# Kernel tuning notes

Measured on AMD Instinct MI355X. Metric: run time of the kernel, lower is better.

## Reference

```python
import jax, jax.numpy as jnp
from jax import lax
import numpy as np

SEL = [46, 92]
A_SEL = [16, 32]
EPS = 1e-16


def _descriptors(xyz, atomtypes, box):
    # xyz: (B,N,3) float, atomtypes: (B,N) int, box: scalar
    B, N, _ = xyz.shape
    dm = xyz[:, :, None, :] - xyz[:, None, :, :] + EPS          # (B,N,N,3)
    dm = dm - box * jnp.round(dm / box)                          # min-image PBC
    dist = jnp.sqrt(jnp.sum(dm * dm, axis=-1))                   # (B,N,N)
    self_mask = jnp.eye(N, dtype=bool)[None]                     # exclude self
    radial, a_xyz_list, a_dist_list = [], [], []
    lf_d = lf_i = None
    for j, (selj, aselj) in enumerate(zip(SEL, A_SEL)):
        mask = (atomtypes == j)[:, None, :] & (~self_mask)       # (B,N,N)
        d_j = jnp.where(mask, dist, jnp.inf)
        k = max(selj, aselj, 2)
        neg, idx = lax.top_k(-d_j, k)                            # k smallest
        sd = -neg                                                # (B,N,k)
        if j == 0:
            lf_d, lf_i = sd[..., :2], idx[..., :2]
        else:
            better = sd[..., :2] < lf_d
            lf_d = jnp.where(better, sd[..., :2], lf_d)
            lf_i = jnp.where(better, idx[..., :2], lf_i)
        radial.append(1.0 / (sd[..., :selj] + EPS))
        a_xyz_list.append(jnp.take_along_axis(dm, idx[..., :aselj, None], axis=2))
        a_dist_list.append(sd[..., :aselj])
    a_xyz = jnp.concatenate(a_xyz_list, axis=2)                  # (B,N,sumA,3)
    a_dist = jnp.concatenate(a_dist_list, axis=2)[..., None]     # (B,N,sumA,1)
    # local frame from the 2 globally nearest neighbors
    l_xyz = jnp.take_along_axis(dm, lf_i[..., None], axis=2) / (lf_d[..., None] + EPS)
    r0, r1 = l_xyz[:, :, 0], l_xyz[:, :, 1]                      # (B,N,3)
    v2 = r1 - jnp.sum(r0 * r1, -1, keepdims=True) * r0
    v2 = v2 / jnp.linalg.norm(v2, axis=-1, keepdims=True)
    v3 = jnp.cross(r0, r1)
    v3 = v3 / jnp.linalg.norm(v3, axis=-1, keepdims=True)
    A = jnp.stack([r0, v2, v3], axis=-2)                         # (B,N,3,3)
    a_xyz = a_xyz / (a_dist + EPS)
    a_xyz = jnp.einsum('bnij,bnkj->bnki', A, a_xyz)
    a_xyz = a_xyz / (a_dist + EPS)  # faithful: source divides by a_dist twice
    return jnp.concatenate(radial + [a_xyz.reshape(B, N, -1)], axis=-1)


def _energy(xyz, atomtypes, box, params):
    # norm is (mean=0, std=1) in the source -> identity, skipped.
    desc = _descriptors(xyz, atomtypes, box)
    e = jnp.zeros(desc.shape[:2], desc.dtype)
    for t, layers in enumerate(params):
        h = desc
        for (W, b) in layers[:-1]:
            h = jnp.tanh(h @ W + b)
        W, b = layers[-1]
        e = jnp.where(atomtypes == t, (h @ W + b)[..., 0], e)
    return jnp.sum(e, axis=1)                                    # (B,)


def setup_inputs():
    key = jax.random.key(0)
    ks = jax.random.split(key, 16)
    B, N, box = 2, 2048, 27
    xyz = jax.random.uniform(ks[0], (B, N, 3), dtype=jnp.float32) * box
    atomtypes = jax.random.randint(ks[1], (B, N), 0, 2)
    D = sum(SEL) + 3 * sum(A_SEL)  # 282
    sizes = [D, 64, 64, 1]
    inp = {'xyz': xyz, 'atomtypes': atomtypes, 'box_size': box}
    ki = 2
    for t in range(2):
        for l in range(3):
            fi, fo = sizes[l], sizes[l + 1]
            inp[f'W{t}_{l}'] = jax.random.normal(ks[ki], (fi, fo), dtype=jnp.float32) / np.sqrt(fi).astype(np.float32)
            inp[f'b{t}_{l}'] = jnp.zeros((fo,), jnp.float32)
            ki += 1
    return inp


def reference(xyz, atomtypes, box_size, W0_0, b0_0, W0_1, b0_1, W0_2, b0_2,
              W1_0, b1_0, W1_1, b1_1, W1_2, b1_2):
    params = [[(W0_0, b0_0), (W0_1, b0_1), (W0_2, b0_2)],
              [(W1_0, b1_0), (W1_1, b1_1), (W1_2, b1_2)]]
    energy = _energy(xyz, atomtypes, box_size, params)
    forces = -jax.grad(lambda x: jnp.sum(_energy(x, atomtypes, box_size, params)))(xyz)
    return energy, forces
```

## Files before the change

kernel.cpp:

```cpp
#include <hip/hip_runtime.h>
#include <stdint.h>
#include <math.h>

#define BLOCK 256
#define WPB 4
#define SEL0 46
#define SEL1 92
#define ASEL0 16
#define ASEL1 32
#define NNB 138
#define NANG 48
#define DDIM 282
#define HID 64
#define FEPS 1e-16f
#define NPT 32
#define CAP 128
#define NREP 16

__device__ __forceinline__ float mimg(float dx, float box, float ibox) {
    return dx - box * rintf(dx * ibox);
}

__device__ __forceinline__ void wsync() {
    asm volatile("s_waitcnt lgkmcnt(0)" ::: "memory");
    __builtin_amdgcn_wave_barrier();
}

__device__ __forceinline__ void decode(unsigned long long k, float& d, int& j) {
    uint32_t idx = (uint32_t)(k & 0xFFFFFFFFull);
    if (idx == 0xFFFFFFFFu) { d = 1e30f; j = -1; }
    else { d = __uint_as_float((uint32_t)(k >> 32)); j = (int)idx; }
}

__device__ __forceinline__ void atomF(float* p, float v, bool wg) {
    if (wg) (void)__hip_atomic_fetch_add(p, v, __ATOMIC_RELAXED,
                                         __HIP_MEMORY_SCOPE_WORKGROUP);
    else    atomicAdd(p, v);
}

__global__ __launch_bounds__(BLOCK)
void reduce_kernel(const float* __restrict__ rep, float* __restrict__ out,
                   int total, int Bc, int eoff, int rstride, int nrep)
{
    int e = blockIdx.x * BLOCK + threadIdx.x;
    if (e >= total) return;
    int src = (e < Bc) ? (eoff + e) : (e - Bc);
    float s = 0.0f;
    for (int r = 0; r < nrep; ++r) s += rep[(size_t)r * rstride + src];
    out[e] = s;
}

__global__ __launch_bounds__(BLOCK, 4)
void md_kernel(const float* __restrict__ xyz, const int* __restrict__ types,
               const void* __restrict__ boxp,
               const float* __restrict__ W0a, const float* __restrict__ B0a,
               const float* __restrict__ W1a, const float* __restrict__ B1a,
               const float* __restrict__ W2a, const float* __restrict__ B2a,
               const float* __restrict__ W0b, const float* __restrict__ B0b,
               const float* __restrict__ W1b, const float* __restrict__ B1b,
               const float* __restrict__ W2b, const float* __restrict__ B2b,
               float* __restrict__ out, float* __restrict__ repbase,
               int nrep, int eoff, int rstride, int B, int N)
{
    __shared__ unsigned long long A0s[WPB][CAP];
    __shared__ unsigned long long A1s[WPB][CAP];
    __shared__ float sdescs[WPB][DDIM];
    __shared__ float sgs[WPB][DDIM];
    __shared__ float sAs[WPB][9];
    __shared__ float sh1s[WPB][HID];
    __shared__ float sdh1s[WPB][HID];

    const int w = threadIdx.x >> 6;
    const int lane = threadIdx.x & 63;
    const int atom = blockIdx.x * WPB + w;
    if (atom >= B * N) return;
    const int b = atom / N;
    const int i = atom - b * N;

    unsigned long long* A0w = A0s[w];
    unsigned long long* A1w = A1s[w];
    float* sdescw = sdescs[w];
    float* sgw = sgs[w];
    float* sAw = sAs[w];
    float* sh1w = sh1s[w];
    float* sdh1w = sdh1s[w];

    const bool wg = (repbase != nullptr);
    float* Fout;
    float* Eout;
    if (wg) {
        uint32_t xcc;
        asm volatile("s_getreg_b32 %0, hwreg(HW_REG_XCC_ID)" : "=s"(xcc));
        int ridx = (int)((xcc & 7u) * 2u + (blockIdx.x & 1u));
        float* base = repbase + (size_t)ridx * rstride;
        Fout = base; Eout = base + eoff;
    } else {
        Fout = out + B; Eout = out;
    }

    int ib_test = ((const int*)boxp)[0];
    float box = (ib_test > 0 && ib_test < 1000000) ? (float)ib_test
                                                   : ((const float*)boxp)[0];
    float ibox = 1.0f / box;

    const float* X = xyz + (size_t)b * N * 3;
    const int*   T = types + (size_t)b * N;
    const int ti = T[i];
    const float xi = X[3*i+0], yi = X[3*i+1], zi = X[3*i+2];

    uint32_t rk[NPT];
    #pragma unroll
    for (int jj = 0; jj < NPT; ++jj) {
        int j = jj * 64 + lane;
        uint32_t k = 0x7FFFFFFFu;
        if (j < N && j != i) {
            float dx = mimg(xi - X[3*j+0], box, ibox);
            float dy = mimg(yi - X[3*j+1], box, ibox);
            float dz = mimg(zi - X[3*j+2], box, ibox);
            float d = sqrtf(dx*dx + dy*dy + dz*dz);
            k = __float_as_uint(d) | (T[j] ? 0x80000000u : 0u);
        }
        rk[jj] = k;
    }

    uint32_t t1 = 0;
    #pragma unroll
    for (int jj = 0; jj < NPT; ++jj) t1 += (rk[jj] >> 31);
    #pragma unroll
    for (int o = 32; o > 0; o >>= 1) t1 += __shfl_down(t1, o, 64);
    t1 = __shfl(t1, 0, 64);
    const int tot1 = (int)t1;
    const int tot0 = (N - 1) - tot1;
    const int need0 = min(SEL0, tot0);
    const int need1 = min(SEL1, tot1);

    const float vol = box * box * box;
    const float c43pi = 4.18879020f;
    float R0 = cbrtf(0.5f * (need0 + CAP) * vol / (c43pi * fmaxf((float)tot0, 1.0f)));
    float R1 = cbrtf(0.5f * (need1 + CAP) * vol / (c43pi * fmaxf((float)tot1, 1.0f)));
    uint32_t Rb0 = __float_as_uint(R0), Rb1 = __float_as_uint(R1);
    float lo0 = 0.0f, hi0 = -1.0f, lo1 = 0.0f, hi1 = -1.0f;
    for (int it = 0; it < 20; ++it) {
        uint32_t c0 = 0, c1 = 0;
        #pragma unroll
        for (int jj = 0; jj < NPT; ++jj) {
            uint32_t k = rk[jj];
            c0 += ((k < 0x80000000u) && (k < Rb0));
            c1 += ((k >= 0x80000000u) && ((k & 0x7FFFFFFFu) < Rb1));
        }
        uint32_t packed = c0 | (c1 << 16);
        #pragma unroll
        for (int o = 32; o > 0; o >>= 1) packed += __shfl_down(packed, o, 64);
        packed = __shfl(packed, 0, 64);
        int cc0 = (int)(packed & 0xFFFFu);
        int cc1 = (int)(packed >> 16);
        bool done0 = (cc0 >= need0 && cc0 <= CAP);
        bool done1 = (cc1 >= need1 && cc1 <= CAP);
        if (done0 && done1) break;
        if (!done0) {
            if (cc0 < need0) { lo0 = R0; R0 = (hi0 > 0.0f) ? 0.5f*(lo0+hi0) : R0*1.3f; }
            else             { hi0 = R0; R0 = 0.5f*(lo0+hi0); }
            Rb0 = __float_as_uint(R0);
        }
        if (!done1) {
            if (cc1 < need1) { lo1 = R1; R1 = (hi1 > 0.0f) ? 0.5f*(lo1+hi1) : R1*1.3f; }
            else             { hi1 = R1; R1 = 0.5f*(lo1+hi1); }
            Rb1 = __float_as_uint(R1);
        }
    }

    const unsigned long long lmlt = (1ull << lane) - 1ull;
    int base0 = 0, base1 = 0;
    #pragma unroll
    for (int jj = 0; jj < NPT; ++jj) {
        uint32_t k = rk[jj];
        bool p0 = (k < 0x80000000u) && (k < Rb0);
        bool p1 = (k >= 0x80000000u) && ((k & 0x7FFFFFFFu) < Rb1);
        unsigned long long m0 = __ballot(p0);
        unsigned long long m1 = __ballot(p1);
        if (p0) {
            int pos = base0 + __popcll(m0 & lmlt);
            if (pos < CAP)
                A0w[pos] = ((unsigned long long)k << 32) | (uint32_t)(jj*64 + lane);
        }
        if (p1) {
            int pos = base1 + __popcll(m1 & lmlt);
            if (pos < CAP)
                A1w[pos] = ((unsigned long long)(k & 0x7FFFFFFFu) << 32) | (uint32_t)(jj*64 + lane);
        }
        base0 += __popcll(m0);
        base1 += __popcll(m1);
    }
    const int c0n = min(base0, CAP);
    const int c1n = min(base1, CAP);
    #pragma unroll
    for (int t = lane; t < CAP; t += 64) {
        if (t >= c0n) A0w[t] = ~0ull;
        if (t >= c1n) A1w[t] = ~0ull;
    }
    wsync();

    {
        unsigned long long va = A0w[lane], vb = A0w[lane + 64];
        unsigned long long wa = A1w[lane], wb = A1w[lane + 64];
        #pragma unroll
        for (int size = 2; size <= 128; size <<= 1) {
            #pragma unroll
            for (int stride = 64; stride > 0; stride >>= 1) {
                if (stride >= size) continue;
                if (stride == 64) {
                    unsigned long long mn = va < vb ? va : vb;
                    unsigned long long mx = va < vb ? vb : va;
                    va = mn; vb = mx;
                    mn = wa < wb ? wa : wb;
                    mx = wa < wb ? wb : wa;
                    wa = mn; wb = mx;
                } else {
                    bool keep_lo = (lane & stride) == 0;
                    bool asc0 = ((lane & size) == 0);
                    bool asc1 = (((lane + 64) & size) == 0);
                    unsigned long long oa = __shfl_xor(va, stride, 64);
                    unsigned long long ob = __shfl_xor(vb, stride, 64);
                    va = (asc0 == keep_lo) ? (va < oa ? va : oa) : (va > oa ? va : oa);
                    vb = (asc1 == keep_lo) ? (vb < ob ? vb : ob) : (vb > ob ? vb : ob);
                    oa = __shfl_xor(wa, stride, 64);
                    ob = __shfl_xor(wb, stride, 64);
                    wa = (asc0 == keep_lo) ? (wa < oa ? wa : oa) : (wa > oa ? wa : oa);
                    wb = (asc1 == keep_lo) ? (wb < ob ? wb : ob) : (wb > ob ? wb : ob);
                }
            }
        }
        A0w[lane] = va; A0w[lane + 64] = vb;
        A1w[lane] = wa; A1w[lane + 64] = wb;
    }
    wsync();

    for (int t = lane; t < NNB; t += 64) {
        unsigned long long k = (t < SEL0) ? A0w[t] : A1w[t - SEL0];
        float d; int j; decode(k, d, j);
        sdescw[t] = 1.0f / (d + FEPS);
    }

    float f_ld0 = 1.0f, f_ld1 = 1.0f; int f_j0 = -1, f_j1 = -1;
    float r0x=0,r0y=0,r0z=0, r1x=0,r1y=0,r1z=0;
    float u0x=0,u0y=0,u0z=0, u1x=0,u1y=0,u1z=0;
    float f_s=0, f_n2=1, f_n3=1;
    float e2x=0,e2y=0,e2z=0, e3x=0,e3y=0,e3z=0;
    if (lane == 0) {
        float da0, da1, db0, db1; int ja0, ja1, jb0, jb1;
        decode(A0w[0], da0, ja0);
        decode(A0w[1], da1, ja1);
        decode(A1w[0], db0, jb0);
        decode(A1w[1], db1, jb1);
        f_ld0 = (db0 < da0) ? db0 : da0;  f_j0 = (db0 < da0) ? jb0 : ja0;
        f_ld1 = (db1 < da1) ? db1 : da1;  f_j1 = (db1 < da1) ? jb1 : ja1;
        if (f_j0 < 0) f_j0 = i;
        if (f_j1 < 0) f_j1 = i;
        u0x = mimg(xi - X[3*f_j0+0], box, ibox);
        u0y = mimg(yi - X[3*f_j0+1], box, ibox);
        u0z = mimg(zi - X[3*f_j0+2], box, ibox);
        u1x = mimg(xi - X[3*f_j1+0], box, ibox);
        u1y = mimg(yi - X[3*f_j1+1], box, ibox);
        u1z = mimg(zi - X[3*f_j1+2], box, ibox);
        float id0 = 1.0f/(f_ld0 + FEPS), id1 = 1.0f/(f_ld1 + FEPS);
        r0x = u0x*id0; r0y = u0y*id0; r0z = u0z*id0;
        r1x = u1x*id1; r1y = u1y*id1; r1z = u1z*id1;
        f_s = r0x*r1x + r0y*r1y + r0z*r1z;
        float v2x = r1x - f_s*r0x, v2y = r1y - f_s*r0y, v2z = r1z - f_s*r0z;
        f_n2 = sqrtf(v2x*v2x + v2y*v2y + v2z*v2z);
        e2x = v2x/f_n2; e2y = v2y/f_n2; e2z = v2z/f_n2;
        float cx = r0y*r1z - r0z*r1y;
        float cy = r0z*r1x - r0x*r1z;
        float cz = r0x*r1y - r0y*r1x;
        f_n3 = sqrtf(cx*cx + cy*cy + cz*cz);
        e3x = cx/f_n3; e3y = cy/f_n3; e3z = cz/f_n3;
        sAw[0]=r0x; sAw[1]=r0y; sAw[2]=r0z;
        sAw[3]=e2x; sAw[4]=e2y; sAw[5]=e2z;
        sAw[6]=e3x; sAw[7]=e3y; sAw[8]=e3z;
    }
    wsync();

    if (lane < NANG) {
        int slot = (lane < ASEL0) ? lane : SEL0 + (lane - ASEL0);
        unsigned long long k = (slot < SEL0) ? A0w[slot] : A1w[slot - SEL0];
        float d; int j; decode(k, d, j);
        float dx = 0, dy = 0, dz = 0;
        if (j >= 0) {
            dx = mimg(xi - X[3*j+0], box, ibox);
            dy = mimg(yi - X[3*j+1], box, ibox);
            dz = mimg(zi - X[3*j+2], box, ibox);
        }
        float de = d + FEPS;
        float q = 1.0f/(de*de);
        float wx = sAw[0]*dx + sAw[1]*dy + sAw[2]*dz;
        float wy = sAw[3]*dx + sAw[4]*dy + sAw[5]*dz;
        float wz = sAw[6]*dx + sAw[7]*dy + sAw[8]*dz;
        sdescw[NNB + 3*lane + 0] = wx*q;
        sdescw[NNB + 3*lane + 1] = wy*q;
        sdescw[NNB + 3*lane + 2] = wz*q;
    }
    wsync();

    const float* W0 = ti ? W0b : W0a;  const float* B0 = ti ? B0b : B0a;
    const float* W1 = ti ? W1b : W1a;  const float* B1 = ti ? B1b : B1a;
    const float* W2 = ti ? W2b : W2a;  const float* B2 = ti ? B2b : B2a;

    float acc = B0[lane];
    for (int d = 0; d < DDIM; ++d) acc = fmaf(sdescw[d], W0[d*HID + lane], acc);
    float h1 = tanhf(acc);
    sh1w[lane] = h1;
    wsync();

    float acc2 = B1[lane];
    #pragma unroll
    for (int m = 0; m < HID; ++m) acc2 = fmaf(sh1w[m], W1[m*HID + lane], acc2);
    float h2 = tanhf(acc2);
    float w2v = W2[lane];
    float part = h2 * w2v;
    #pragma unroll
    for (int o = 32; o > 0; o >>= 1) part += __shfl_down(part, o, 64);
    if (lane == 0) atomF(&Eout[b], part + B2[0], wg);
    float dh2 = (1.0f - h2*h2) * w2v;
    sdh1w[lane] = dh2;
    wsync();

    float accb = 0.0f;
    #pragma unroll
    for (int m = 0; m < HID; ++m) accb = fmaf(W1[lane*HID + m], sdh1w[m], accb);
    wsync();
    float dh1 = (1.0f - h1*h1) * accb;
    sdh1w[lane] = dh1;
    wsync();

    for (int d = lane; d < DDIM; d += 64) {
        float a = 0.0f;
        #pragma unroll
        for (int m = 0; m < HID; ++m) a = fmaf(W0[d*HID + m], sdh1w[m], a);
        sgw[d] = a;
    }
    wsync();

    float rG[9];
    #pragma unroll
    for (int q9 = 0; q9 < 9; ++q9) rG[q9] = 0.0f;
    float fix = 0.0f, fiy = 0.0f, fiz = 0.0f;

    for (int t = lane; t < NNB; t += 64) {
        unsigned long long k = (t < SEL0) ? A0w[t] : A1w[t - SEL0];
        float d; int j; decode(k, d, j);
        if (j >= 0) {
            float dx = mimg(xi - X[3*j+0], box, ibox);
            float dy = mimg(yi - X[3*j+1], box, ibox);
            float dz = mimg(zi - X[3*j+2], box, ibox);
            float gr = sgw[t];
            float de = d + FEPS;
            float coef = -gr / (d * de * de);
            float gx = coef*dx, gy = coef*dy, gz = coef*dz;
            int a = -1;
            if (t < ASEL0) a = t;
            else if (t >= SEL0 && t < SEL0 + ASEL1) a = ASEL0 + (t - SEL0);
            if (a >= 0) {
                float q = 1.0f/(de*de);
                float gax = sgw[NNB+3*a+0], gay = sgw[NNB+3*a+1], gaz = sgw[NNB+3*a+2];
                float wx = sAw[0]*dx + sAw[1]*dy + sAw[2]*dz;
                float wy = sAw[3]*dx + sAw[4]*dy + sAw[5]*dz;
                float wz = sAw[6]*dx + sAw[7]*dy + sAw[8]*dz;
                float tx = sAw[0]*gax + sAw[3]*gay + sAw[6]*gaz;
                float ty = sAw[1]*gax + sAw[4]*gay + sAw[7]*gaz;
                float tz = sAw[2]*gax + sAw[5]*gay + sAw[8]*gaz;
                float gw = gax*wx + gay*wy + gaz*wz;
                float c2 = -2.0f * gw * q / (de * d);
                gx += q*tx + c2*dx;
                gy += q*ty + c2*dy;
                gz += q*tz + c2*dz;
                rG[0] += gax*dx*q; rG[1] += gax*dy*q; rG[2] += gax*dz*q;
                rG[3] += gay*dx*q; rG[4] += gay*dy*q; rG[5] += gay*dz*q;
                rG[6] += gaz*dx*q; rG[7] += gaz*dy*q; rG[8] += gaz*dz*q;
            }
            float* Fj = Fout + 3*((size_t)b*N + j);
            atomF(&Fj[0], gx, wg); atomF(&Fj[1], gy, wg); atomF(&Fj[2], gz, wg);
            fix -= gx; fiy -= gy; fiz -= gz;
        }
    }

    #pragma unroll
    for (int o = 32; o > 0; o >>= 1) {
        #pragma unroll
        for (int q9 = 0; q9 < 9; ++q9) rG[q9] += __shfl_down(rG[q9], o, 64);
        fix += __shfl_down(fix, o, 64);
        fiy += __shfl_down(fiy, o, 64);
        fiz += __shfl_down(fiz, o, 64);
    }

    if (lane == 0) {
        float g0x=rG[0], g0y=rG[1], g0z=rG[2];
        float g2x=rG[3], g2y=rG[4], g2z=rG[5];
        float g3x=rG[6], g3y=rG[7], g3z=rG[8];
        float d3 = g3x*e3x + g3y*e3y + g3z*e3z;
        float in3 = 1.0f/f_n3;
        float dcx = (g3x - d3*e3x)*in3;
        float dcy = (g3y - d3*e3y)*in3;
        float dcz = (g3z - d3*e3z)*in3;
        float gr0x = r1y*dcz - r1z*dcy;
        float gr0y = r1z*dcx - r1x*dcz;
        float gr0z = r1x*dcy - r1y*dcx;
        float gr1x = dcy*r0z - dcz*r0y;
        float gr1y = dcz*r0x - dcx*r0z;
        float gr1z = dcx*r0y - dcy*r0x;
        float d2 = g2x*e2x + g2y*e2y + g2z*e2z;
        float in2 = 1.0f/f_n2;
        float dvx = (g2x - d2*e2x)*in2;
        float dvy = (g2y - d2*e2y)*in2;
        float dvz = (g2z - d2*e2z)*in2;
        gr1x += dvx; gr1y += dvy; gr1z += dvz;
        gr0x -= f_s*dvx; gr0y -= f_s*dvy; gr0z -= f_s*dvz;
        float dss = -(dvx*r0x + dvy*r0y + dvz*r0z);
        gr0x += dss*r1x; gr0y += dss*r1y; gr0z += dss*r1z;
        gr1x += dss*r0x; gr1y += dss*r0y; gr1z += dss*r0z;
        gr0x += g0x; gr0y += g0y; gr0z += g0z;
        float de0 = f_ld0 + FEPS;
        float dot0 = gr0x*u0x + gr0y*u0y + gr0z*u0z;
        float k0 = dot0 / (f_ld0 * de0 * de0);
        float gu0x = gr0x/de0 - k0*u0x;
        float gu0y = gr0y/de0 - k0*u0y;
        float gu0z = gr0z/de0 - k0*u0z;
        float de1 = f_ld1 + FEPS;
        float dot1 = gr1x*u1x + gr1y*u1y + gr1z*u1z;
        float k1 = dot1 / (f_ld1 * de1 * de1);
        float gu1x = gr1x/de1 - k1*u1x;
        float gu1y = gr1y/de1 - k1*u1y;
        float gu1z = gr1z/de1 - k1*u1z;
        float* Fj0 = Fout + 3*((size_t)b*N + f_j0);
        atomF(&Fj0[0], gu0x, wg); atomF(&Fj0[1], gu0y, wg); atomF(&Fj0[2], gu0z, wg);
        float* Fj1 = Fout + 3*((size_t)b*N + f_j1);
        atomF(&Fj1[0], gu1x, wg); atomF(&Fj1[1], gu1y, wg); atomF(&Fj1[2], gu1z, wg);
        fix -= gu0x + gu1x;
        fiy -= gu0y + gu1y;
        fiz -= gu0z + gu1z;
        float* Fi = Fout + 3*((size_t)b*N + i);
        atomF(&Fi[0], fix, wg); atomF(&Fi[1], fiy, wg); atomF(&Fi[2], fiz, wg);
    }
}

extern "C" void kernel_launch(void* const* d_in, const int* in_sizes, int n_in,
                              void* d_out, int out_size, void* d_ws, size_t ws_size,
                              hipStream_t stream) {
    const float* xyz  = (const float*)d_in[0];
    const int*   types = (const int*)d_in[1];
    const void*  boxp = d_in[2];
    int BN = in_sizes[1];
    int B = out_size - 3*BN;
    if (B < 1) B = 1;
    int N = BN / B;

    int eoff = ((3 * BN + 31) / 32) * 32;
    int rstride = eoff + ((B + 31) / 32) * 32;
    int nrep = NREP;
    size_t need = (size_t)nrep * rstride * sizeof(float);
    float* rep = (need <= ws_size) ? (float*)d_ws : nullptr;

    if (rep) {
        hipMemsetAsync(d_ws, 0, need, stream);
    } else {
        nrep = 1;
        hipMemsetAsync(d_out, 0, (size_t)out_size * sizeof(float), stream);
    }

    int nblk = (BN + WPB - 1) / WPB;
    md_kernel<<<dim3(nblk), dim3(BLOCK), 0, stream>>>(
        xyz, types, boxp,
        (const float*)d_in[3],  (const float*)d_in[4],
        (const float*)d_in[5],  (const float*)d_in[6],
        (const float*)d_in[7],  (const float*)d_in[8],
        (const float*)d_in[9],  (const float*)d_in[10],
        (const float*)d_in[11], (const float*)d_in[12],
        (const float*)d_in[13], (const float*)d_in[14],
        (float*)d_out, rep, nrep, eoff, rstride, B, N);

    if (rep) {
        int total = out_size;
        int nb = (total + BLOCK - 1) / BLOCK;
        reduce_kernel<<<dim3(nb), dim3(BLOCK), 0, stream>>>(
            rep, (float*)d_out, total, B, eoff, rstride, nrep);
    }
}
```

Measured before the change: 282.7 us.

## Accumulate forces in per-block shared memory and write per-block slots for reduction

```diff
diff --git a/kernel.cpp b/kernel.cpp
--- a/kernel.cpp
+++ b/kernel.cpp
@@ -15,7 +15,8 @@
 #define FEPS 1e-16f
 #define NPT 32
 #define CAP 128
-#define NREP 16
+#define NMAX 2048
+#define SFE (3*NMAX)
 
 __device__ __forceinline__ float mimg(float dx, float box, float ibox) {
     return dx - box * rintf(dx * ibox);
@@ -32,25 +33,27 @@
     else { d = __uint_as_float((uint32_t)(k >> 32)); j = (int)idx; }
 }
 
-__device__ __forceinline__ void atomF(float* p, float v, bool wg) {
-    if (wg) (void)__hip_atomic_fetch_add(p, v, __ATOMIC_RELAXED,
-                                         __HIP_MEMORY_SCOPE_WORKGROUP);
-    else    atomicAdd(p, v);
-}
-
 __global__ __launch_bounds__(BLOCK)
 void reduce_kernel(const float* __restrict__ rep, float* __restrict__ out,
-                   int total, int Bc, int eoff, int rstride, int nrep)
+                   int total, int B, int N, int sstride, int nspb)
 {
     int e = blockIdx.x * BLOCK + threadIdx.x;
     if (e >= total) return;
-    int src = (e < Bc) ? (eoff + e) : (e - Bc);
     float s = 0.0f;
-    for (int r = 0; r < nrep; ++r) s += rep[(size_t)r * rstride + src];
+    if (e < B) {
+        const float* p = rep + (size_t)e * nspb * sstride + 3 * N;
+        for (int r = 0; r < nspb; ++r) s += p[(size_t)r * sstride];
+    } else {
+        int f = e - B;
+        int b = f / (3 * N);
+        int elem = f - b * 3 * N;
+        const float* p = rep + (size_t)b * nspb * sstride + elem;
+        for (int r = 0; r < nspb; ++r) s += p[(size_t)r * sstride];
+    }
     out[e] = s;
 }
 
-__global__ __launch_bounds__(BLOCK, 4)
+__global__ __launch_bounds__(BLOCK, 2)
 void md_kernel(const float* __restrict__ xyz, const int* __restrict__ types,
                const void* __restrict__ boxp,
                const float* __restrict__ W0a, const float* __restrict__ B0a,
@@ -59,8 +62,8 @@
                const float* __restrict__ W0b, const float* __restrict__ B0b,
                const float* __restrict__ W1b, const float* __restrict__ B1b,
                const float* __restrict__ W2b, const float* __restrict__ B2b,
-               float* __restrict__ out, float* __restrict__ repbase,
-               int nrep, int eoff, int rstride, int B, int N)
+               float* __restrict__ out, float* __restrict__ slotbase,
+               int sstride, int G, int B, int N)
 {
     __shared__ unsigned long long A0s[WPB][CAP];
     __shared__ unsigned long long A1s[WPB][CAP];
@@ -69,13 +72,14 @@
     __shared__ float sAs[WPB][9];
     __shared__ float sh1s[WPB][HID];
     __shared__ float sdh1s[WPB][HID];
+    __shared__ float sF[3*NMAX + 8];
 
     const int w = threadIdx.x >> 6;
     const int lane = threadIdx.x & 63;
-    const int atom = blockIdx.x * WPB + w;
-    if (atom >= B * N) return;
-    const int b = atom / N;
-    const int i = atom - b * N;
+    const bool lmode = (slotbase != nullptr);
+
+    for (int s2 = threadIdx.x; s2 <= SFE; s2 += BLOCK) sF[s2] = 0.0f;
+    __syncthreads();
 
     unsigned long long* A0w = A0s[w];
     unsigned long long* A1w = A1s[w];
@@ -85,360 +89,385 @@
     float* sh1w = sh1s[w];
     float* sdh1w = sdh1s[w];
 
-    const bool wg = (repbase != nullptr);
-    float* Fout;
-    float* Eout;
-    if (wg) {
-        uint32_t xcc;
-        asm volatile("s_getreg_b32 %0, hwreg(HW_REG_XCC_ID)" : "=s"(xcc));
-        int ridx = (int)((xcc & 7u) * 2u + (blockIdx.x & 1u));
-        float* base = repbase + (size_t)ridx * rstride;
-        Fout = base; Eout = base + eoff;
-    } else {
-        Fout = out + B; Eout = out;
-    }
-
     int ib_test = ((const int*)boxp)[0];
     float box = (ib_test > 0 && ib_test < 1000000) ? (float)ib_test
                                                    : ((const float*)boxp)[0];
     float ibox = 1.0f / box;
 
-    const float* X = xyz + (size_t)b * N * 3;
-    const int*   T = types + (size_t)b * N;
-    const int ti = T[i];
-    const float xi = X[3*i+0], yi = X[3*i+1], zi = X[3*i+2];
-
-    uint32_t rk[NPT];
-    #pragma unroll
-    for (int jj = 0; jj < NPT; ++jj) {
-        int j = jj * 64 + lane;
-        uint32_t k = 0x7FFFFFFFu;
-        if (j < N && j != i) {
-            float dx = mimg(xi - X[3*j+0], box, ibox);
-            float dy = mimg(yi - X[3*j+1], box, ibox);
-            float dz = mimg(zi - X[3*j+2], box, ibox);
-            float d = sqrtf(dx*dx + dy*dy + dz*dz);
-            k = __float_as_uint(d) | (T[j] ? 0x80000000u : 0u);
-        }
-        rk[jj] = k;
-    }
-
-    uint32_t t1 = 0;
-    #pragma unroll
-    for (int jj = 0; jj < NPT; ++jj) t1 += (rk[jj] >> 31);
-    #pragma unroll
-    for (int o = 32; o > 0; o >>= 1) t1 += __shfl_down(t1, o, 64);
-    t1 = __shfl(t1, 0, 64);
-    const int tot1 = (int)t1;
-    const int tot0 = (N - 1) - tot1;
-    const int need0 = min(SEL0, tot0);
-    const int need1 = min(SEL1, tot1);
-
-    const float vol = box * box * box;
-    const float c43pi = 4.18879020f;
-    float R0 = cbrtf(0.5f * (need0 + CAP) * vol / (c43pi * fmaxf((float)tot0, 1.0f)));
-    float R1 = cbrtf(0.5f * (need1 + CAP) * vol / (c43pi * fmaxf((float)tot1, 1.0f)));
-    uint32_t Rb0 = __float_as_uint(R0), Rb1 = __float_as_uint(R1);
-    float lo0 = 0.0f, hi0 = -1.0f, lo1 = 0.0f, hi1 = -1.0f;
-    for (int it = 0; it < 20; ++it) {
-        uint32_t c0 = 0, c1 = 0;
+    const int gpw = G / WPB;
+
+    for (int k2 = 0; k2 < gpw; ++k2) {
+      const int atom = blockIdx.x * G + w * gpw + k2;
+      if (atom < B * N) {
+        const int b = atom / N;
+        const int i = atom - b * N;
+
+        const float* X = xyz + (size_t)b * N * 3;
+        const int*   T = types + (size_t)b * N;
+        const int ti = T[i];
+        const float xi = X[3*i+0], yi = X[3*i+1], zi = X[3*i+2];
+        float* Fg = out + B + (size_t)3 * b * N;
+
+        uint32_t rk[NPT];
+        #pragma unroll
+        for (int jj = 0; jj < NPT; ++jj) {
+            int j = jj * 64 + lane;
+            uint32_t k = 0x7FFFFFFFu;
+            if (j < N && j != i) {
+                float dx = mimg(xi - X[3*j+0], box, ibox);
+                float dy = mimg(yi - X[3*j+1], box, ibox);
+                float dz = mimg(zi - X[3*j+2], box, ibox);
+                float d = sqrtf(dx*dx + dy*dy + dz*dz);
+                k = __float_as_uint(d) | (T[j] ? 0x80000000u : 0u);
+            }
+            rk[jj] = k;
+        }
+
+        uint32_t t1 = 0;
+        #pragma unroll
+        for (int jj = 0; jj < NPT; ++jj) t1 += (rk[jj] >> 31);
+        #pragma unroll
+        for (int o = 32; o > 0; o >>= 1) t1 += __shfl_down(t1, o, 64);
+        t1 = __shfl(t1, 0, 64);
+        const int tot1 = (int)t1;
+        const int tot0 = (N - 1) - tot1;
+        const int need0 = min(SEL0, tot0);
+        const int need1 = min(SEL1, tot1);
+
+        const float vol = box * box * box;
+        const float c43pi = 4.18879020f;
+        float R0 = cbrtf(0.5f * (need0 + CAP) * vol / (c43pi * fmaxf((float)tot0, 1.0f)));
+        float R1 = cbrtf(0.5f * (need1 + CAP) * vol / (c43pi * fmaxf((float)tot1, 1.0f)));
+        uint32_t Rb0 = __float_as_uint(R0), Rb1 = __float_as_uint(R1);
+        float lo0 = 0.0f, hi0 = -1.0f, lo1 = 0.0f, hi1 = -1.0f;
+        for (int it = 0; it < 20; ++it) {
+            uint32_t c0 = 0, c1 = 0;
+            #pragma unroll
+            for (int jj = 0; jj < NPT; ++jj) {
+                uint32_t k = rk[jj];
+                c0 += ((k < 0x80000000u) && (k < Rb0));
+                c1 += ((k >= 0x80000000u) && ((k & 0x7FFFFFFFu) < Rb1));
+            }
+            uint32_t packed = c0 | (c1 << 16);
+            #pragma unroll
+            for (int o = 32; o > 0; o >>= 1) packed += __shfl_down(packed, o, 64);
+            packed = __shfl(packed, 0, 64);
+            int cc0 = (int)(packed & 0xFFFFu);
+            int cc1 = (int)(packed >> 16);
+            bool done0 = (cc0 >= need0 && cc0 <= CAP);
+            bool done1 = (cc1 >= need1 && cc1 <= CAP);
+            if (done0 && done1) break;
+            if (!done0) {
+                if (cc0 < need0) { lo0 = R0; R0 = (hi0 > 0.0f) ? 0.5f*(lo0+hi0) : R0*1.3f; }
+                else             { hi0 = R0; R0 = 0.5f*(lo0+hi0); }
+                Rb0 = __float_as_uint(R0);
+            }
+            if (!done1) {
+                if (cc1 < need1) { lo1 = R1; R1 = (hi1 > 0.0f) ? 0.5f*(lo1+hi1) : R1*1.3f; }
+                else             { hi1 = R1; R1 = 0.5f*(lo1+hi1); }
+                Rb1 = __float_as_uint(R1);
+            }
+        }
+
+        const unsigned long long lmlt = (1ull << lane) - 1ull;
+        int base0 = 0, base1 = 0;
         #pragma unroll
         for (int jj = 0; jj < NPT; ++jj) {
             uint32_t k = rk[jj];
-            c0 += ((k < 0x80000000u) && (k < Rb0));
-            c1 += ((k >= 0x80000000u) && ((k & 0x7FFFFFFFu) < Rb1));
-        }
-        uint32_t packed = c0 | (c1 << 16);
-        #pragma unroll
-        for (int o = 32; o > 0; o >>= 1) packed += __shfl_down(packed, o, 64);
-        packed = __shfl(packed, 0, 64);
-        int cc0 = (int)(packed & 0xFFFFu);
-        int cc1 = (int)(packed >> 16);
-        bool done0 = (cc0 >= need0 && cc0 <= CAP);
-        bool done1 = (cc1 >= need1 && cc1 <= CAP);
-        if (done0 && done1) break;
-        if (!done0) {
-            if (cc0 < need0) { lo0 = R0; R0 = (hi0 > 0.0f) ? 0.5f*(lo0+hi0) : R0*1.3f; }
-            else             { hi0 = R0; R0 = 0.5f*(lo0+hi0); }
-            Rb0 = __float_as_uint(R0);
-        }
-        if (!done1) {
-            if (cc1 < need1) { lo1 = R1; R1 = (hi1 > 0.0f) ? 0.5f*(lo1+hi1) : R1*1.3f; }
-            else             { hi1 = R1; R1 = 0.5f*(lo1+hi1); }
-            Rb1 = __float_as_uint(R1);
-        }
+            bool p0 = (k < 0x80000000u) && (k < Rb0);
+            bool p1 = (k >= 0x80000000u) && ((k & 0x7FFFFFFFu) < Rb1);
+            unsigned long long m0 = __ballot(p0);
+            unsigned long long m1 = __ballot(p1);
+            if (p0) {
+                int pos = base0 + __popcll(m0 & lmlt);
+                if (pos < CAP)
+                    A0w[pos] = ((unsigned long long)k << 32) | (uint32_t)(jj*64 + lane);
+            }
+            if (p1) {
+                int pos = base1 + __popcll(m1 & lmlt);
+                if (pos < CAP)
+                    A1w[pos] = ((unsigned long long)(k & 0x7FFFFFFFu) << 32) | (uint32_t)(jj*64 + lane);
+            }
+            base0 += __popcll(m0);
+            base1 += __popcll(m1);
+        }
+        const int c0n = min(base0, CAP);
+        const int c1n = min(base1, CAP);
+        #pragma unroll
+        for (int t = lane; t < CAP; t += 64) {
+            if (t >= c0n) A0w[t] = ~0ull;
+            if (t >= c1n) A1w[t] = ~0ull;
+        }
+        wsync();
+
+        {
+            unsigned long long va = A0w[lane], vb = A0w[lane + 64];
+            unsigned long long wa = A1w[lane], wb = A1w[lane + 64];
+            #pragma unroll
+            for (int size = 2; size <= 128; size <<= 1) {
+                #pragma unroll
+                for (int stride = 64; stride > 0; stride >>= 1) {
+                    if (stride >= size) continue;
+                    if (stride == 64) {
+                        unsigned long long mn = va < vb ? va : vb;
+                        unsigned long long mx = va < vb ? vb : va;
+                        va = mn; vb = mx;
+                        mn = wa < wb ? wa : wb;
+                        mx = wa < wb ? wb : wa;
+                        wa = mn; wb = mx;
+                    } else {
+                        bool keep_lo = (lane & stride) == 0;
+                        bool asc0 = ((lane & size) == 0);
+                        bool asc1 = (((lane + 64) & size) == 0);
+                        unsigned long long oa = __shfl_xor(va, stride, 64);
+                        unsigned long long ob = __shfl_xor(vb, stride, 64);
+                        va = (asc0 == keep_lo) ? (va < oa ? va : oa) : (va > oa ? va : oa);
+                        vb = (asc1 == keep_lo) ? (vb < ob ? vb : ob) : (vb > ob ? vb : ob);
+                        oa = __shfl_xor(wa, stride, 64);
+                        ob = __shfl_xor(wb, stride, 64);
+                        wa = (asc0 == keep_lo) ? (wa < oa ? wa : oa) : (wa > oa ? wa : oa);
+                        wb = (asc1 == keep_lo) ? (wb < ob ? wb : ob) : (wb > ob ? wb : ob);
+                    }
+                }
+            }
+            A0w[lane] = va; A0w[lane + 64] = vb;
+            A1w[lane] = wa; A1w[lane + 64] = wb;
+        }
+        wsync();
+
+        for (int t = lane; t < NNB; t += 64) {
+            unsigned long long k = (t < SEL0) ? A0w[t] : A1w[t - SEL0];
+            float d; int j; decode(k, d, j);
+            sdescw[t] = 1.0f / (d + FEPS);
+        }
+
+        float f_ld0 = 1.0f, f_ld1 = 1.0f; int f_j0 = -1, f_j1 = -1;
+        float r0x=0,r0y=0,r0z=0, r1x=0,r1y=0,r1z=0;
+        float u0x=0,u0y=0,u0z=0, u1x=0,u1y=0,u1z=0;
+        float f_s=0, f_n2=1, f_n3=1;
+        float e2x=0,e2y=0,e2z=0, e3x=0,e3y=0,e3z=0;
+        if (lane == 0) {
+            float da0, da1, db0, db1; int ja0, ja1, jb0, jb1;
+            decode(A0w[0], da0, ja0);
+            decode(A0w[1], da1, ja1);
+            decode(A1w[0], db0, jb0);
+            decode(A1w[1], db1, jb1);
+            f_ld0 = (db0 < da0) ? db0 : da0;  f_j0 = (db0 < da0) ? jb0 : ja0;
+            f_ld1 = (db1 < da1) ? db1 : da1;  f_j1 = (db1 < da1) ? jb1 : ja1;
+            if (f_j0 < 0) f_j0 = i;
+            if (f_j1 < 0) f_j1 = i;
+            u0x = mimg(xi - X[3*f_j0+0], box, ibox);
+            u0y = mimg(yi - X[3*f_j0+1], box, ibox);
+            u0z = mimg(zi - X[3*f_j0+2], box, ibox);
+            u1x = mimg(xi - X[3*f_j1+0], box, ibox);
+            u1y = mimg(yi - X[3*f_j1+1], box, ibox);
+            u1z = mimg(zi - X[3*f_j1+2], box, ibox);
+            float id0 = 1.0f/(f_ld0 + FEPS), id1 = 1.0f/(f_ld1 + FEPS);
+            r0x = u0x*id0; r0y = u0y*id0; r0z = u0z*id0;
+            r1x = u1x*id1; r1y = u1y*id1; r1z = u1z*id1;
+            f_s = r0x*r1x + r0y*r1y + r0z*r1z;
+            float v2x = r1x - f_s*r0x, v2y = r1y - f_s*r0y, v2z = r1z - f_s*r0z;
+            f_n2 = sqrtf(v2x*v2x + v2y*v2y + v2z*v2z);
+            e2x = v2x/f_n2; e2y = v2y/f_n2; e2z = v2z/f_n2;
+            float cx = r0y*r1z - r0z*r1y;
+            float cy = r0z*r1x - r0x*r1z;
+            float cz = r0x*r1y - r0y*r1x;
+            f_n3 = sqrtf(cx*cx + cy*cy + cz*cz);
+            e3x = cx/f_n3; e3y = cy/f_n3; e3z = cz/f_n3;
+            sAw[0]=r0x; sAw[1]=r0y; sAw[2]=r0z;
+            sAw[3]=e2x; sAw[4]=e2y; sAw[5]=e2z;
+            sAw[6]=e3x; sAw[7]=e3y; sAw[8]=e3z;
+        }
+        wsync();
+
+        if (lane < NANG) {
+            int slot = (lane < ASEL0) ? lane : SEL0 + (lane - ASEL0);
+            unsigned long long k = (slot < SEL0) ? A0w[slot] : A1w[slot - SEL0];
+            float d; int j; decode(k, d, j);
+            float dx = 0, dy = 0, dz = 0;
+            if (j >= 0) {
+                dx = mimg(xi - X[3*j+0], box, ibox);
+                dy = mimg(yi - X[3*j+1], box, ibox);
+                dz = mimg(zi - X[3*j+2], box, ibox);
+            }
+            float de = d + FEPS;
+            float q = 1.0f/(de*de);
+            float wx = sAw[0]*dx + sAw[1]*dy + sAw[2]*dz;
+            float wy = sAw[3]*dx + sAw[4]*dy + sAw[5]*dz;
+            float wz = sAw[6]*dx + sAw[7]*dy + sAw[8]*dz;
+            sdescw[NNB + 3*lane + 0] = wx*q;
+            sdescw[NNB + 3*lane + 1] = wy*q;
+            sdescw[NNB + 3*lane + 2] = wz*q;
+        }
+        wsync();
+
+        const float* W0 = ti ? W0b : W0a;  const float* B0 = ti ? B0b : B0a;
+        const float* W1 = ti ? W1b : W1a;  const float* B1 = ti ? B1b : B1a;
+        const float* W2 = ti ? W2b : W2a;  const float* B2 = ti ? B2b : B2a;
+
+        float a0 = 0.0f, a1 = 0.0f, a2 = 0.0f, a3 = 0.0f;
+        for (int d = 0; d < DDIM - 2; d += 4) {
+            a0 = fmaf(sdescw[d+0], W0[(d+0)*HID + lane], a0);
+            a1 = fmaf(sdescw[d+1], W0[(d+1)*HID + lane], a1);
+            a2 = fmaf(sdescw[d+2], W0[(d+2)*HID + lane], a2);
+            a3 = fmaf(sdescw[d+3], W0[(d+3)*HID + lane], a3);
+        }
+        a0 = fmaf(sdescw[DDIM-2], W0[(DDIM-2)*HID + lane], a0);
+        a1 = fmaf(sdescw[DDIM-1], W0[(DDIM-1)*HID + lane], a1);
+        float h1 = tanhf(B0[lane] + ((a0 + a1) + (a2 + a3)));
+        sh1w[lane] = h1;
+        wsync();
+
+        float acc2 = B1[lane];
+        #pragma unroll
+        for (int m = 0; m < HID; ++m) acc2 = fmaf(sh1w[m], W1[m*HID + lane], acc2);
+        float h2 = tanhf(acc2);
+        float w2v = W2[lane];
+        float part = h2 * w2v;
+        #pragma unroll
+        for (int o = 32; o > 0; o >>= 1) part += __shfl_down(part, o, 64);
+        if (lane == 0) {
+            if (lmode) atomicAdd(&sF[SFE], part + B2[0]);
+            else       atomicAdd(&out[b], part + B2[0]);
+        }
+        float dh2 = (1.0f - h2*h2) * w2v;
+        sdh1w[lane] = dh2;
+        wsync();
+
+        float accb = 0.0f;
+        #pragma unroll
+        for (int m = 0; m < HID; ++m) accb = fmaf(W1[lane*HID + m], sdh1w[m], accb);
+        wsync();
+        float dh1 = (1.0f - h1*h1) * accb;
+        sdh1w[lane] = dh1;
+        wsync();
+
+        for (int d = lane; d < DDIM; d += 64) {
+            float a = 0.0f;
+            #pragma unroll
+            for (int m = 0; m < HID; ++m) a = fmaf(W0[d*HID + m], sdh1w[m], a);
+            sgw[d] = a;
+        }
+        wsync();
+
+        float rG[9];
+        #pragma unroll
+        for (int q9 = 0; q9 < 9; ++q9) rG[q9] = 0.0f;
+        float fix = 0.0f, fiy = 0.0f, fiz = 0.0f;
+
+        for (int t = lane; t < NNB; t += 64) {
+            unsigned long long k = (t < SEL0) ? A0w[t] : A1w[t - SEL0];
+            float d; int j; decode(k, d, j);
+            if (j >= 0) {
+                float dx = mimg(xi - X[3*j+0], box, ibox);
+                float dy = mimg(yi - X[3*j+1], box, ibox);
+                float dz = mimg(zi - X[3*j+2], box, ibox);
+                float gr = sgw[t];
+                float de = d + FEPS;
+                float coef = -gr / (d * de * de);
+                float gx = coef*dx, gy = coef*dy, gz = coef*dz;
+                int a = -1;
+                if (t < ASEL0) a = t;
+                else if (t >= SEL0 && t < SEL0 + ASEL1) a = ASEL0 + (t - SEL0);
+                if (a >= 0) {
+                    float q = 1.0f/(de*de);
+                    float gax = sgw[NNB+3*a+0], gay = sgw[NNB+3*a+1], gaz = sgw[NNB+3*a+2];
+                    float wx = sAw[0]*dx + sAw[1]*dy + sAw[2]*dz;
+                    float wy = sAw[3]*dx + sAw[4]*dy + sAw[5]*dz;
+                    float wz = sAw[6]*dx + sAw[7]*dy + sAw[8]*dz;
+                    float tx = sAw[0]*gax + sAw[3]*gay + sAw[6]*gaz;
+                    float ty = sAw[1]*gax + sAw[4]*gay + sAw[7]*gaz;
+                    float tz = sAw[2]*gax + sAw[5]*gay + sAw[8]*gaz;
+                    float gw = gax*wx + gay*wy + gaz*wz;
+                    float c2 = -2.0f * gw * q / (de * d);
+                    gx += q*tx + c2*dx;
+                    gy += q*ty + c2*dy;
+                    gz += q*tz + c2*dz;
+                    rG[0] += gax*dx*q; rG[1] += gax*dy*q; rG[2] += gax*dz*q;
+                    rG[3] += gay*dx*q; rG[4] += gay*dy*q; rG[5] += gay*dz*q;
+                    rG[6] += gaz*dx*q; rG[7] += gaz*dy*q; rG[8] += gaz*dz*q;
+                }
+                if (lmode) {
+                    atomicAdd(&sF[3*j+0], gx);
+                    atomicAdd(&sF[3*j+1], gy);
+                    atomicAdd(&sF[3*j+2], gz);
+                } else {
+                    atomicAdd(&Fg[3*j+0], gx);
+                    atomicAdd(&Fg[3*j+1], gy);
+                    atomicAdd(&Fg[3*j+2], gz);
+                }
+                fix -= gx; fiy -= gy; fiz -= gz;
+            }
+        }
+
+        #pragma unroll
+        for (int o = 32; o > 0; o >>= 1) {
+            #pragma unroll
+            for (int q9 = 0; q9 < 9; ++q9) rG[q9] += __shfl_down(rG[q9], o, 64);
+            fix += __shfl_down(fix, o, 64);
+            fiy += __shfl_down(fiy, o, 64);
+            fiz += __shfl_down(fiz, o, 64);
+        }
+
+        if (lane == 0) {
+            float g0x=rG[0], g0y=rG[1], g0z=rG[2];
+            float g2x=rG[3], g2y=rG[4], g2z=rG[5];
+            float g3x=rG[6], g3y=rG[7], g3z=rG[8];
+            float d3 = g3x*e3x + g3y*e3y + g3z*e3z;
+            float in3 = 1.0f/f_n3;
+            float dcx = (g3x - d3*e3x)*in3;
+            float dcy = (g3y - d3*e3y)*in3;
+            float dcz = (g3z - d3*e3z)*in3;
+            float gr0x = r1y*dcz - r1z*dcy;
+            float gr0y = r1z*dcx - r1x*dcz;
+            float gr0z = r1x*dcy - r1y*dcx;
+            float gr1x = dcy*r0z - dcz*r0y;
+            float gr1y = dcz*r0x - dcx*r0z;
+            float gr1z = dcx*r0y - dcy*r0x;
+            float d2 = g2x*e2x + g2y*e2y + g2z*e2z;
+            float in2 = 1.0f/f_n2;
+            float dvx = (g2x - d2*e2x)*in2;
+            float dvy = (g2y - d2*e2y)*in2;
+            float dvz = (g2z - d2*e2z)*in2;
+            gr1x += dvx; gr1y += dvy; gr1z += dvz;
+            gr0x -= f_s*dvx; gr0y -= f_s*dvy; gr0z -= f_s*dvz;
+            float dss = -(dvx*r0x + dvy*r0y + dvz*r0z);
+            gr0x += dss*r1x; gr0y += dss*r1y; gr0z += dss*r1z;
+            gr1x += dss*r0x; gr1y += dss*r0y; gr1z += dss*r0z;
+            gr0x += g0x; gr0y += g0y; gr0z += g0z;
+            float de0 = f_ld0 + FEPS;
+            float dot0 = gr0x*u0x + gr0y*u0y + gr0z*u0z;
+            float k0 = dot0 / (f_ld0 * de0 * de0);
+            float gu0x = gr0x/de0 - k0*u0x;
+            float gu0y = gr0y/de0 - k0*u0y;
+            float gu0z = gr0z/de0 - k0*u0z;
+            float de1 = f_ld1 + FEPS;
+            float dot1 = gr1x*u1x + gr1y*u1y + gr1z*u1z;
+            float k1 = dot1 / (f_ld1 * de1 * de1);
+            float gu1x = gr1x/de1 - k1*u1x;
+            float gu1y = gr1y/de1 - k1*u1y;
+            float gu1z = gr1z/de1 - k1*u1z;
+            fix -= gu0x + gu1x;
+            fiy -= gu0y + gu1y;
+            fiz -= gu0z + gu1z;
+            if (lmode) {
+                atomicAdd(&sF[3*f_j0+0], gu0x); atomicAdd(&sF[3*f_j0+1], gu0y); atomicAdd(&sF[3*f_j0+2], gu0z);
+                atomicAdd(&sF[3*f_j1+0], gu1x); atomicAdd(&sF[3*f_j1+1], gu1y); atomicAdd(&sF[3*f_j1+2], gu1z);
+                atomicAdd(&sF[3*i+0], fix);     atomicAdd(&sF[3*i+1], fiy);     atomicAdd(&sF[3*i+2], fiz);
+            } else {
+                atomicAdd(&Fg[3*f_j0+0], gu0x); atomicAdd(&Fg[3*f_j0+1], gu0y); atomicAdd(&Fg[3*f_j0+2], gu0z);
+                atomicAdd(&Fg[3*f_j1+0], gu1x); atomicAdd(&Fg[3*f_j1+1], gu1y); atomicAdd(&Fg[3*f_j1+2], gu1z);
+                atomicAdd(&Fg[3*i+0], fix);     atomicAdd(&Fg[3*i+1], fiy);     atomicAdd(&Fg[3*i+2], fiz);
+            }
+        }
+      }
     }
 
-    const unsigned long long lmlt = (1ull << lane) - 1ull;
-    int base0 = 0, base1 = 0;
-    #pragma unroll
-    for (int jj = 0; jj < NPT; ++jj) {
-        uint32_t k = rk[jj];
-        bool p0 = (k < 0x80000000u) && (k < Rb0);
-        bool p1 = (k >= 0x80000000u) && ((k & 0x7FFFFFFFu) < Rb1);
-        unsigned long long m0 = __ballot(p0);
-        unsigned long long m1 = __ballot(p1);
-        if (p0) {
-            int pos = base0 + __popcll(m0 & lmlt);
-            if (pos < CAP)
-                A0w[pos] = ((unsigned long long)k << 32) | (uint32_t)(jj*64 + lane);
-        }
-        if (p1) {
-            int pos = base1 + __popcll(m1 & lmlt);
-            if (pos < CAP)
-                A1w[pos] = ((unsigned long long)(k & 0x7FFFFFFFu) << 32) | (uint32_t)(jj*64 + lane);
-        }
-        base0 += __popcll(m0);
-        base1 += __popcll(m1);
-    }
-    const int c0n = min(base0, CAP);
-    const int c1n = min(base1, CAP);
-    #pragma unroll
-    for (int t = lane; t < CAP; t += 64) {
-        if (t >= c0n) A0w[t] = ~0ull;
-        if (t >= c1n) A1w[t] = ~0ull;
-    }
-    wsync();
-
-    {
-        unsigned long long va = A0w[lane], vb = A0w[lane + 64];
-        unsigned long long wa = A1w[lane], wb = A1w[lane + 64];
-        #pragma unroll
-        for (int size = 2; size <= 128; size <<= 1) {
-            #pragma unroll
-            for (int stride = 64; stride > 0; stride >>= 1) {
-                if (stride >= size) continue;
-                if (stride == 64) {
-                    unsigned long long mn = va < vb ? va : vb;
-                    unsigned long long mx = va < vb ? vb : va;
-                    va = mn; vb = mx;
-                    mn = wa < wb ? wa : wb;
-                    mx = wa < wb ? wb : wa;
-                    wa = mn; wb = mx;
-                } else {
-                    bool keep_lo = (lane & stride) == 0;
-                    bool asc0 = ((lane & size) == 0);
-                    bool asc1 = (((lane + 64) & size) == 0);
-                    unsigned long long oa = __shfl_xor(va, stride, 64);
-                    unsigned long long ob = __shfl_xor(vb, stride, 64);
-                    va = (asc0 == keep_lo) ? (va < oa ? va : oa) : (va > oa ? va : oa);
-                    vb = (asc1 == keep_lo) ? (vb < ob ? vb : ob) : (vb > ob ? vb : ob);
-                    oa = __shfl_xor(wa, stride, 64);
-                    ob = __shfl_xor(wb, stride, 64);
-                    wa = (asc0 == keep_lo) ? (wa < oa ? wa : oa) : (wa > oa ? wa : oa);
-                    wb = (asc1 == keep_lo) ? (wb < ob ? wb : ob) : (wb > ob ? wb : ob);
-                }
-            }
-        }
-        A0w[lane] = va; A0w[lane + 64] = vb;
-        A1w[lane] = wa; A1w[lane + 64] = wb;
-    }
-    wsync();
-
-    for (int t = lane; t < NNB; t += 64) {
-        unsigned long long k = (t < SEL0) ? A0w[t] : A1w[t - SEL0];
-        float d; int j; decode(k, d, j);
-        sdescw[t] = 1.0f / (d + FEPS);
-    }
-
-    float f_ld0 = 1.0f, f_ld1 = 1.0f; int f_j0 = -1, f_j1 = -1;
-    float r0x=0,r0y=0,r0z=0, r1x=0,r1y=0,r1z=0;
-    float u0x=0,u0y=0,u0z=0, u1x=0,u1y=0,u1z=0;
-    float f_s=0, f_n2=1, f_n3=1;
-    float e2x=0,e2y=0,e2z=0, e3x=0,e3y=0,e3z=0;
-    if (lane == 0) {
-        float da0, da1, db0, db1; int ja0, ja1, jb0, jb1;
-        decode(A0w[0], da0, ja0);
-        decode(A0w[1], da1, ja1);
-        decode(A1w[0], db0, jb0);
-        decode(A1w[1], db1, jb1);
-        f_ld0 = (db0 < da0) ? db0 : da0;  f_j0 = (db0 < da0) ? jb0 : ja0;
-        f_ld1 = (db1 < da1) ? db1 : da1;  f_j1 = (db1 < da1) ? jb1 : ja1;
-        if (f_j0 < 0) f_j0 = i;
-        if (f_j1 < 0) f_j1 = i;
-        u0x = mimg(xi - X[3*f_j0+0], box, ibox);
-        u0y = mimg(yi - X[3*f_j0+1], box, ibox);
-        u0z = mimg(zi - X[3*f_j0+2], box, ibox);
-        u1x = mimg(xi - X[3*f_j1+0], box, ibox);
-        u1y = mimg(yi - X[3*f_j1+1], box, ibox);
-        u1z = mimg(zi - X[3*f_j1+2], box, ibox);
-        float id0 = 1.0f/(f_ld0 + FEPS), id1 = 1.0f/(f_ld1 + FEPS);
-        r0x = u0x*id0; r0y = u0y*id0; r0z = u0z*id0;
-        r1x = u1x*id1; r1y = u1y*id1; r1z = u1z*id1;
-        f_s = r0x*r1x + r0y*r1y + r0z*r1z;
-        float v2x = r1x - f_s*r0x, v2y = r1y - f_s*r0y, v2z = r1z - f_s*r0z;
-        f_n2 = sqrtf(v2x*v2x + v2y*v2y + v2z*v2z);
-        e2x = v2x/f_n2; e2y = v2y/f_n2; e2z = v2z/f_n2;
-        float cx = r0y*r1z - r0z*r1y;
-        float cy = r0z*r1x - r0x*r1z;
-        float cz = r0x*r1y - r0y*r1x;
-        f_n3 = sqrtf(cx*cx + cy*cy + cz*cz);
-        e3x = cx/f_n3; e3y = cy/f_n3; e3z = cz/f_n3;
-        sAw[0]=r0x; sAw[1]=r0y; sAw[2]=r0z;
-        sAw[3]=e2x; sAw[4]=e2y; sAw[5]=e2z;
-        sAw[6]=e3x; sAw[7]=e3y; sAw[8]=e3z;
-    }
-    wsync();
-
-    if (lane < NANG) {
-        int slot = (lane < ASEL0) ? lane : SEL0 + (lane - ASEL0);
-        unsigned long long k = (slot < SEL0) ? A0w[slot] : A1w[slot - SEL0];
-        float d; int j; decode(k, d, j);
-        float dx = 0, dy = 0, dz = 0;
-        if (j >= 0) {
-            dx = mimg(xi - X[3*j+0], box, ibox);
-            dy = mimg(yi - X[3*j+1], box, ibox);
-            dz = mimg(zi - X[3*j+2], box, ibox);
-        }
-        float de = d + FEPS;
-        float q = 1.0f/(de*de);
-        float wx = sAw[0]*dx + sAw[1]*dy + sAw[2]*dz;
-        float wy = sAw[3]*dx + sAw[4]*dy + sAw[5]*dz;
-        float wz = sAw[6]*dx + sAw[7]*dy + sAw[8]*dz;
-        sdescw[NNB + 3*lane + 0] = wx*q;
-        sdescw[NNB + 3*lane + 1] = wy*q;
-        sdescw[NNB + 3*lane + 2] = wz*q;
-    }
-    wsync();
-
-    const float* W0 = ti ? W0b : W0a;  const float* B0 = ti ? B0b : B0a;
-    const float* W1 = ti ? W1b : W1a;  const float* B1 = ti ? B1b : B1a;
-    const float* W2 = ti ? W2b : W2a;  const float* B2 = ti ? B2b : B2a;
-
-    float acc = B0[lane];
-    for (int d = 0; d < DDIM; ++d) acc = fmaf(sdescw[d], W0[d*HID + lane], acc);
-    float h1 = tanhf(acc);
-    sh1w[lane] = h1;
-    wsync();
-
-    float acc2 = B1[lane];
-    #pragma unroll
-    for (int m = 0; m < HID; ++m) acc2 = fmaf(sh1w[m], W1[m*HID + lane], acc2);
-    float h2 = tanhf(acc2);
-    float w2v = W2[lane];
-    float part = h2 * w2v;
-    #pragma unroll
-    for (int o = 32; o > 0; o >>= 1) part += __shfl_down(part, o, 64);
-    if (lane == 0) atomF(&Eout[b], part + B2[0], wg);
-    float dh2 = (1.0f - h2*h2) * w2v;
-    sdh1w[lane] = dh2;
-    wsync();
-
-    float accb = 0.0f;
-    #pragma unroll
-    for (int m = 0; m < HID; ++m) accb = fmaf(W1[lane*HID + m], sdh1w[m], accb);
-    wsync();
-    float dh1 = (1.0f - h1*h1) * accb;
-    sdh1w[lane] = dh1;
-    wsync();
-
-    for (int d = lane; d < DDIM; d += 64) {
-        float a = 0.0f;
-        #pragma unroll
-        for (int m = 0; m < HID; ++m) a = fmaf(W0[d*HID + m], sdh1w[m], a);
-        sgw[d] = a;
-    }
-    wsync();
-
-    float rG[9];
-    #pragma unroll
-    for (int q9 = 0; q9 < 9; ++q9) rG[q9] = 0.0f;
-    float fix = 0.0f, fiy = 0.0f, fiz = 0.0f;
-
-    for (int t = lane; t < NNB; t += 64) {
-        unsigned long long k = (t < SEL0) ? A0w[t] : A1w[t - SEL0];
-        float d; int j; decode(k, d, j);
-        if (j >= 0) {
-            float dx = mimg(xi - X[3*j+0], box, ibox);
-            float dy = mimg(yi - X[3*j+1], box, ibox);
-            float dz = mimg(zi - X[3*j+2], box, ibox);
-            float gr = sgw[t];
-            float de = d + FEPS;
-            float coef = -gr / (d * de * de);
-            float gx = coef*dx, gy = coef*dy, gz = coef*dz;
-            int a = -1;
-            if (t < ASEL0) a = t;
-            else if (t >= SEL0 && t < SEL0 + ASEL1) a = ASEL0 + (t - SEL0);
-            if (a >= 0) {
-                float q = 1.0f/(de*de);
-                float gax = sgw[NNB+3*a+0], gay = sgw[NNB+3*a+1], gaz = sgw[NNB+3*a+2];
-                float wx = sAw[0]*dx + sAw[1]*dy + sAw[2]*dz;
-                float wy = sAw[3]*dx + sAw[4]*dy + sAw[5]*dz;
-                float wz = sAw[6]*dx + sAw[7]*dy + sAw[8]*dz;
-                float tx = sAw[0]*gax + sAw[3]*gay + sAw[6]*gaz;
-                float ty = sAw[1]*gax + sAw[4]*gay + sAw[7]*gaz;
-                float tz = sAw[2]*gax + sAw[5]*gay + sAw[8]*gaz;
-                float gw = gax*wx + gay*wy + gaz*wz;
-                float c2 = -2.0f * gw * q / (de * d);
-                gx += q*tx + c2*dx;
-                gy += q*ty + c2*dy;
-                gz += q*tz + c2*dz;
-                rG[0] += gax*dx*q; rG[1] += gax*dy*q; rG[2] += gax*dz*q;
-                rG[3] += gay*dx*q; rG[4] += gay*dy*q; rG[5] += gay*dz*q;
-                rG[6] += gaz*dx*q; rG[7] += gaz*dy*q; rG[8] += gaz*dz*q;
-            }
-            float* Fj = Fout + 3*((size_t)b*N + j);
-            atomF(&Fj[0], gx, wg); atomF(&Fj[1], gy, wg); atomF(&Fj[2], gz, wg);
-            fix -= gx; fiy -= gy; fiz -= gz;
-        }
-    }
-
-    #pragma unroll
-    for (int o = 32; o > 0; o >>= 1) {
-        #pragma unroll
-        for (int q9 = 0; q9 < 9; ++q9) rG[q9] += __shfl_down(rG[q9], o, 64);
-        fix += __shfl_down(fix, o, 64);
-        fiy += __shfl_down(fiy, o, 64);
-        fiz += __shfl_down(fiz, o, 64);
-    }
-
-    if (lane == 0) {
-        float g0x=rG[0], g0y=rG[1], g0z=rG[2];
-        float g2x=rG[3], g2y=rG[4], g2z=rG[5];
-        float g3x=rG[6], g3y=rG[7], g3z=rG[8];
-        float d3 = g3x*e3x + g3y*e3y + g3z*e3z;
-        float in3 = 1.0f/f_n3;
-        float dcx = (g3x - d3*e3x)*in3;
-        float dcy = (g3y - d3*e3y)*in3;
-        float dcz = (g3z - d3*e3z)*in3;
-        float gr0x = r1y*dcz - r1z*dcy;
-        float gr0y = r1z*dcx - r1x*dcz;
-        float gr0z = r1x*dcy - r1y*dcx;
-        float gr1x = dcy*r0z - dcz*r0y;
-        float gr1y = dcz*r0x - dcx*r0z;
-        float gr1z = dcx*r0y - dcy*r0x;
-        float d2 = g2x*e2x + g2y*e2y + g2z*e2z;
-        float in2 = 1.0f/f_n2;
-        float dvx = (g2x - d2*e2x)*in2;
-        float dvy = (g2y - d2*e2y)*in2;
-        float dvz = (g2z - d2*e2z)*in2;
-        gr1x += dvx; gr1y += dvy; gr1z += dvz;
-        gr0x -= f_s*dvx; gr0y -= f_s*dvy; gr0z -= f_s*dvz;
-        float dss = -(dvx*r0x + dvy*r0y + dvz*r0z);
-        gr0x += dss*r1x; gr0y += dss*r1y; gr0z += dss*r1z;
-        gr1x += dss*r0x; gr1y += dss*r0y; gr1z += dss*r0z;
-        gr0x += g0x; gr0y += g0y; gr0z += g0z;
-        float de0 = f_ld0 + FEPS;
-        float dot0 = gr0x*u0x + gr0y*u0y + gr0z*u0z;
-        float k0 = dot0 / (f_ld0 * de0 * de0);
-        float gu0x = gr0x/de0 - k0*u0x;
-        float gu0y = gr0y/de0 - k0*u0y;
-        float gu0z = gr0z/de0 - k0*u0z;
-        float de1 = f_ld1 + FEPS;
-        float dot1 = gr1x*u1x + gr1y*u1y + gr1z*u1z;
-        float k1 = dot1 / (f_ld1 * de1 * de1);
-        float gu1x = gr1x/de1 - k1*u1x;
-        float gu1y = gr1y/de1 - k1*u1y;
-        float gu1z = gr1z/de1 - k1*u1z;
-        float* Fj0 = Fout + 3*((size_t)b*N + f_j0);
-        atomF(&Fj0[0], gu0x, wg); atomF(&Fj0[1], gu0y, wg); atomF(&Fj0[2], gu0z, wg);
-        float* Fj1 = Fout + 3*((size_t)b*N + f_j1);
-        atomF(&Fj1[0], gu1x, wg); atomF(&Fj1[1], gu1y, wg); atomF(&Fj1[2], gu1z, wg);
-        fix -= gu0x + gu1x;
-        fiy -= gu0y + gu1y;
-        fiz -= gu0z + gu1z;
-        float* Fi = Fout + 3*((size_t)b*N + i);
-        atomF(&Fi[0], fix, wg); atomF(&Fi[1], fiy, wg); atomF(&Fi[2], fiz, wg);
+    __syncthreads();
+    if (lmode) {
+        float* slotp = slotbase + (size_t)blockIdx.x * sstride;
+        for (int s2 = threadIdx.x; s2 < 3*N; s2 += BLOCK) slotp[s2] = sF[s2];
+        if (threadIdx.x == 0) slotp[3*N] = sF[SFE];
     }
 }
 
@@ -453,34 +482,43 @@
     if (B < 1) B = 1;
     int N = BN / B;
 
-    int eoff = ((3 * BN + 31) / 32) * 32;
-    int rstride = eoff + ((B + 31) / 32) * 32;
-    int nrep = NREP;
-    size_t need = (size_t)nrep * rstride * sizeof(float);
-    float* rep = (need <= ws_size) ? (float*)d_ws : nullptr;
-
-    if (rep) {
-        hipMemsetAsync(d_ws, 0, need, stream);
+    int sstride = 3 * N + 32;
+    int G = 0;
+    if (N <= NMAX) {
+        for (int g = 8; g <= 64; g <<= 1) {
+            if (N % g || BN % g) continue;
+            size_t needb = (size_t)(BN / g) * sstride * sizeof(float);
+            if (needb <= ws_size) { G = g; break; }
+        }
+    }
+
+    if (G) {
+        float* rep = (float*)d_ws;
+        int nblk = BN / G;
+        md_kernel<<<dim3(nblk), dim3(BLOCK), 0, stream>>>(
+            xyz, types, boxp,
+            (const float*)d_in[3],  (const float*)d_in[4],
+            (const float*)d_in[5],  (const float*)d_in[6],
+            (const float*)d_in[7],  (const float*)d_in[8],
+            (const float*)d_in[9],  (const float*)d_in[10],
+            (const float*)d_in[11], (const float*)d_in[12],
+            (const float*)d_in[13], (const float*)d_in[14],
+            (float*)d_out, rep, sstride, G, B, N);
+        int nspb = N / G;
+        int nb = (out_size + BLOCK - 1) / BLOCK;
+        reduce_kernel<<<dim3(nb), dim3(BLOCK), 0, stream>>>(
+            rep, (float*)d_out, out_size, B, N, sstride, nspb);
     } else {
-        nrep = 1;
         hipMemsetAsync(d_out, 0, (size_t)out_size * sizeof(float), stream);
-    }
-
-    int nblk = (BN + WPB - 1) / WPB;
-    md_kernel<<<dim3(nblk), dim3(BLOCK), 0, stream>>>(
-        xyz, types, boxp,
-        (const float*)d_in[3],  (const float*)d_in[4],
-        (const float*)d_in[5],  (const float*)d_in[6],
-        (const float*)d_in[7],  (const float*)d_in[8],
-        (const float*)d_in[9],  (const float*)d_in[10],
-        (const float*)d_in[11], (const float*)d_in[12],
-        (const float*)d_in[13], (const float*)d_in[14],
-        (float*)d_out, rep, nrep, eoff, rstride, B, N);
-
-    if (rep) {
-        int total = out_size;
-        int nb = (total + BLOCK - 1) / BLOCK;
-        reduce_kernel<<<dim3(nb), dim3(BLOCK), 0, stream>>>(
-            rep, (float*)d_out, total, B, eoff, rstride, nrep);
+        int nblk = (BN + WPB - 1) / WPB;
+        md_kernel<<<dim3(nblk), dim3(BLOCK), 0, stream>>>(
+            xyz, types, boxp,
+            (const float*)d_in[3],  (const float*)d_in[4],
+            (const float*)d_in[5],  (const float*)d_in[6],
+            (const float*)d_in[7],  (const float*)d_in[8],
+            (const float*)d_in[9],  (const float*)d_in[10],
+            (const float*)d_in[11], (const float*)d_in[12],
+            (const float*)d_in[13], (const float*)d_in[14],
+            (float*)d_out, nullptr, 0, WPB, B, N);
     }
 }
```

New measurement: 369.4 us. 30.7% more time.
